# Kernel optimization log

Hardware: AMD Instinct MI355X
Metric: run time of the kernel (lower is better)

Reference implementation:

```python
import jax, jax.numpy as jnp
import numpy as np

N, C, H, E = 10000, 128, 256, 320000
CUTOFF = 5.0
EPS = 1e-5


def _ln(x, g, b):
    mu = jnp.mean(x, axis=-1, keepdims=True)
    var = jnp.var(x, axis=-1, keepdims=True)
    return (x - mu) * jax.lax.rsqrt(var + EPS) * g + b


def setup_inputs() -> dict:
    key = jax.random.key(0)
    ks = jax.random.split(key, 24)

    def w(k, shape, fan_in):
        return (jax.random.normal(k, shape, dtype=jnp.float32) / np.sqrt(fan_in)).astype(jnp.float32)

    inp = {}
    inp["x"] = jax.random.normal(ks[0], (N, 3), dtype=jnp.float32)
    inp["h"] = jax.random.normal(ks[1], (N, C), dtype=jnp.float32)
    inp["edge_index"] = jax.random.randint(ks[2], (2, E), 0, N, dtype=jnp.int32)
    # edge_mlp: Linear(2C+1 -> H), SiLU, Linear(H -> H), SiLU
    inp["We1"] = w(ks[3], (2 * C + 1, H), 2 * C + 1); inp["be1"] = jnp.zeros((H,), jnp.float32)
    inp["We2"] = w(ks[4], (H, H), H);                inp["be2"] = jnp.zeros((H,), jnp.float32)
    # node_mlp: Linear(C+H -> H), SiLU, Linear(H -> C)
    inp["Wn1"] = w(ks[5], (C + H, H), C + H);        inp["bn1"] = jnp.zeros((H,), jnp.float32)
    inp["Wn2"] = w(ks[6], (H, C), H);                inp["bn2"] = jnp.zeros((C,), jnp.float32)
    # residual mlp: Linear(C -> H), SiLU, Dropout(eval), Linear(H -> C)
    inp["Wm1"] = w(ks[7], (C, H), C);                inp["bm1"] = jnp.zeros((H,), jnp.float32)
    inp["Wm2"] = w(ks[8], (H, C), H);                inp["bm2"] = jnp.zeros((C,), jnp.float32)
    # layernorms
    inp["g1"] = jnp.ones((C,), jnp.float32); inp["beta1"] = jnp.zeros((C,), jnp.float32)
    inp["g2"] = jnp.ones((C,), jnp.float32); inp["beta2"] = jnp.zeros((C,), jnp.float32)
    return inp


def reference(x, h, edge_index, We1, be1, We2, be2, Wn1, bn1, Wn2, bn2,
              Wm1, bm1, Wm2, bm2, g1, beta1, g2, beta2):
    row, col = edge_index[0], edge_index[1]

    h_res = h
    hn = _ln(h, g1, beta1)                              # [N, C]

    # ---- EGNN layer ----
    rel = x[row] - x[col]                               # [E, 3]
    dist = jnp.linalg.norm(rel, axis=-1, keepdims=True) # [E, 1]
    edge_in = jnp.concatenate([hn[row], hn[col], dist], axis=-1)  # [E, 2C+1]
    m = jax.nn.silu(edge_in @ We1 + be1)
    m = jax.nn.silu(m @ We2 + be2)                      # [E, H]

    d = dist[:, 0]
    Ccut = 0.5 * (jnp.cos(d * jnp.pi / CUTOFF) + 1.0)
    Ccut = Ccut * (d <= CUTOFF) * (d >= 0.0)
    m = m * Ccut[:, None]

    # mean-aggregate messages at target nodes (edge_index[1])
    sums = jax.ops.segment_sum(m, col, num_segments=N)          # [N, H]
    cnt = jax.ops.segment_sum(jnp.ones((m.shape[0],), m.dtype), col, num_segments=N)
    m_aggr = sums / jnp.maximum(cnt, 1.0)[:, None]

    hd = jax.nn.silu(jnp.concatenate([hn, m_aggr], axis=-1) @ Wn1 + bn1) @ Wn2 + bn2
    h_egnn = hn + hd

    h1 = h_res + h_egnn

    # ---- norm2 + MLP residual (dropout = identity in eval) ----
    h2 = _ln(h1, g2, beta2)
    h2 = jax.nn.silu(h2 @ Wm1 + bm1) @ Wm2 + bm2
    return h1 + h2
```

## Files before the change

### kernel.cpp

```cpp
#include <hip/hip_runtime.h>

#define NN 10000
#define CC 128
#define HH 256
#define EE 320000
#define ETILE 128
#define EBLOCKS 2500

typedef __bf16 bf16_t;
typedef __bf16 bf16x8 __attribute__((ext_vector_type(8)));
typedef __bf16 bf16x4 __attribute__((ext_vector_type(4)));
typedef float f32x4 __attribute__((ext_vector_type(4)));

__device__ __forceinline__ float silu_f(float v) {
#if __has_builtin(__builtin_amdgcn_rcpf)
  return v * __builtin_amdgcn_rcpf(1.0f + __expf(-v));
#else
  return v / (1.0f + __expf(-v));
#endif
}

template<int RE, int KD, int SA, int NT>
__device__ __forceinline__ void gemm_lg(const bf16_t* sAa, const bf16_t* __restrict__ BT,
                                        int nwavebase, int lr, int quad, f32x4 acc[RE][NT]) {
  for (int kk = 0; kk < KD; kk += 32) {
    bf16x8 a[RE]; bf16x8 b[NT];
#pragma unroll
    for (int re = 0; re < RE; re++)
      a[re] = *(const bf16x8*)(sAa + (re * 16 + lr) * SA + kk + quad * 8);
#pragma unroll
    for (int ce = 0; ce < NT; ce++)
      b[ce] = *(const bf16x8*)(BT + (size_t)(nwavebase + ce * 16 + lr) * KD + kk + quad * 8);
#pragma unroll
    for (int re = 0; re < RE; re++)
#pragma unroll
      for (int ce = 0; ce < NT; ce++)
        acc[re][ce] = __builtin_amdgcn_mfma_f32_16x16x32_bf16(a[re], b[ce], acc[re][ce], 0, 0, 0);
  }
}

__global__ __launch_bounds__(256) void prep_kernel(
    const float* __restrict__ We1, const float* __restrict__ We2,
    const float* __restrict__ Wn1, const float* __restrict__ Wn2,
    const float* __restrict__ Wm1, const float* __restrict__ Wm2,
    bf16_t* __restrict__ We1T, bf16_t* __restrict__ We2T,
    bf16_t* __restrict__ Wn1T, bf16_t* __restrict__ Wn2T,
    bf16_t* __restrict__ Wm1T, bf16_t* __restrict__ Wm2T) {
  int i = blockIdx.x * 256 + threadIdx.x;
  if (i < 327680) {
    const float* src; bf16_t* dst; int K, Nc, idx;
    if      (i < 65536)  { src = We1; dst = We1T; K = 256; Nc = 256; idx = i; }
    else if (i < 131072) { src = We2; dst = We2T; K = 256; Nc = 256; idx = i - 65536; }
    else if (i < 229376) { src = Wn1; dst = Wn1T; K = 384; Nc = 256; idx = i - 131072; }
    else if (i < 262144) { src = Wn2; dst = Wn2T; K = 256; Nc = 128; idx = i - 229376; }
    else if (i < 294912) { src = Wm1; dst = Wm1T; K = 128; Nc = 256; idx = i - 262144; }
    else                 { src = Wm2; dst = Wm2T; K = 256; Nc = 128; idx = i - 294912; }
    int n = idx / K, k = idx - n * K;
    dst[idx] = (bf16_t)src[(size_t)k * Nc + n];
  }
}

__global__ __launch_bounds__(256, 4) void node_pre_kernel(
    const float* __restrict__ h, const float* __restrict__ g1,
    const float* __restrict__ bt1,
    const bf16_t* __restrict__ We1T, const float* __restrict__ be1,
    bf16_t* __restrict__ hn16, bf16_t* __restrict__ PQ,
    const int* __restrict__ ei, int* __restrict__ cnt) {
  __shared__ __align__(16) bf16_t sHn[16 * 136];
  int tid = threadIdx.x;
  if (blockIdx.x >= 625) {
    int e = (blockIdx.x - 625) * 256 + tid;
    atomicAdd(&cnt[ei[EE + e]], 1);
    return;
  }
  int lane = tid & 63, wave = tid >> 6;
  int lr = lane & 15, quad = lane >> 4;
  int n0 = blockIdx.x * 16;

  {
    int node = tid >> 4, c0 = (tid & 15) * 8;
    size_t base = (size_t)(n0 + node) * CC;
    f32x4 u0 = *(const f32x4*)(h + base + c0);
    f32x4 u1 = *(const f32x4*)(h + base + c0 + 4);
    float s = 0.f, sq = 0.f;
#pragma unroll
    for (int j = 0; j < 4; j++) { s += u0[j] + u1[j]; sq += u0[j] * u0[j] + u1[j] * u1[j]; }
#pragma unroll
    for (int o = 8; o > 0; o >>= 1) { s += __shfl_xor(s, o); sq += __shfl_xor(sq, o); }
    float mu = s * (1.0f / CC);
    float var = sq * (1.0f / CC) - mu * mu;
    float rs = rsqrtf(var + 1e-5f);
    f32x4 gg0 = *(const f32x4*)(g1 + c0), gg1 = *(const f32x4*)(g1 + c0 + 4);
    f32x4 bb0 = *(const f32x4*)(bt1 + c0), bb1 = *(const f32x4*)(bt1 + c0 + 4);
    bf16x8 ov;
#pragma unroll
    for (int j = 0; j < 4; j++) {
      ov[j] = (bf16_t)((u0[j] - mu) * rs * gg0[j] + bb0[j]);
      ov[j + 4] = (bf16_t)((u1[j] - mu) * rs * gg1[j] + bb1[j]);
    }
    *(bf16x8*)(sHn + node * 136 + c0) = ov;
    *(bf16x8*)(hn16 + base + c0) = ov;
  }
  __syncthreads();

  bool isQ = wave >= 2;
  int rbase = (wave & 1) * 128;
  int koff = isQ ? 128 : 0;
  f32x4 zf = {0.f, 0.f, 0.f, 0.f};
  f32x4 acc[8];
#pragma unroll
  for (int i = 0; i < 8; i++) acc[i] = zf;
  for (int kk = 0; kk < 128; kk += 32) {
    bf16x8 b = *(const bf16x8*)(sHn + lr * 136 + kk + quad * 8);
    bf16x8 a[8];
#pragma unroll
    for (int re = 0; re < 8; re++)
      a[re] = *(const bf16x8*)(We1T + (size_t)(rbase + re * 16 + lr) * 256 + koff + kk + quad * 8);
#pragma unroll
    for (int re = 0; re < 8; re++)
      acc[re] = __builtin_amdgcn_mfma_f32_16x16x32_bf16(a[re], b, acc[re], 0, 0, 0);
  }
#pragma unroll
  for (int re = 0; re < 8; re++) {
    int cb = rbase + re * 16 + quad * 4;
    f32x4 bb = isQ ? zf : *(const f32x4*)(be1 + cb);
    bf16x4 o;
#pragma unroll
    for (int r = 0; r < 4; r++) o[r] = (bf16_t)(acc[re][r] + bb[r]);
    *(bf16x4*)(PQ + (size_t)(n0 + lr) * 512 + (isQ ? 256 : 0) + cb) = o;
  }
}

__global__ __launch_bounds__(1024) void scan_kernel(const int* __restrict__ cnt, int* __restrict__ cursor) {
  __shared__ int wsum[16];
  int tid = threadIdx.x, wave = tid >> 6, lane = tid & 63;
  int base = tid * 10;
  int v[10]; int S = 0;
#pragma unroll
  for (int j = 0; j < 10; j++) {
    int i = base + j;
    v[j] = (i < NN) ? cnt[i] : 0;
    S += v[j];
  }
  int s = S;
#pragma unroll
  for (int off = 1; off < 64; off <<= 1) { int t = __shfl_up(s, off); if (lane >= off) s += t; }
  if (lane == 63) wsum[wave] = s;
  __syncthreads();
  if (tid < 16) {
    int ws = wsum[tid];
#pragma unroll
    for (int off = 1; off < 16; off <<= 1) { int t = __shfl_up(ws, off); if (tid >= off) ws += t; }
    wsum[tid] = ws;
  }
  __syncthreads();
  int ex = ((wave > 0) ? wsum[wave - 1] : 0) + s - S;
#pragma unroll
  for (int j = 0; j < 10; j++) {
    int i = base + j;
    if (i < NN) cursor[i] = ex;
    ex += v[j];
  }
}

__global__ __launch_bounds__(256) void scatter_kernel(const int* __restrict__ ei,
                                                      const float* __restrict__ x,
                                                      int* __restrict__ cursor,
                                                      uint4* __restrict__ edat) {
  int e = blockIdx.x * 256 + threadIdx.x;
  int r = ei[e], c = ei[EE + e];
  float dx = x[3 * r] - x[3 * c];
  float dy = x[3 * r + 1] - x[3 * c + 1];
  float dz = x[3 * r + 2] - x[3 * c + 2];
  float d = sqrtf(dx * dx + dy * dy + dz * dz);
  float cc = (d <= 5.0f) ? 0.5f * (__cosf(d * 0.6283185307179586f) + 1.0f) : 0.0f;
  int pos = atomicAdd(&cursor[c], 1);
  uint4 v = {(unsigned)r, (unsigned)c, __float_as_uint(d), __float_as_uint(cc)};
  edat[pos] = v;
}

__global__ __launch_bounds__(512, 4) void edge_mlp_kernel(
    const uint4* __restrict__ edat, const bf16_t* __restrict__ PQ,
    const float* __restrict__ We1last,
    const bf16_t* __restrict__ We2T, const float* __restrict__ be2,
    float* __restrict__ sums) {
  __shared__ __align__(512) bf16_t sM1[ETILE * 256];
  __shared__ int sRow[ETILE], sCol[ETILE];
  __shared__ float sD[ETILE], sCc[ETILE];
  __shared__ unsigned long long sMaskA, sMaskB;
  int tid = threadIdx.x;
  int lane = tid & 63, wave = tid >> 6;
  int lr = lane & 15, quad = lane >> 4;

  int bid = blockIdx.x;
  int xcd = bid & 7, rank = bid >> 3;
  int swz = (xcd < 4 ? xcd * 313 : 4 * 313 + (xcd - 4) * 312) + rank;
  int e0 = swz * ETILE;

  if (tid < ETILE) {
    uint4 v = edat[e0 + tid];
    sRow[tid] = (int)v.x; sCol[tid] = (int)v.y;
    sD[tid] = __uint_as_float(v.z); sCc[tid] = __uint_as_float(v.w);
  }
  __syncthreads();

  if (tid < ETILE) {
    int fl = (tid > 0) && (sCol[tid] != sCol[tid - 1]);
    unsigned long long m = __ballot(fl);
    if (tid == 0) sMaskA = m;
    if (tid == 64) sMaskB = m;
  }

#pragma unroll
  for (int i = 0; i < 8; i++) {
    int o = tid + i * 512;
    int e = o >> 5, q = o & 31;
    int k0 = q * 8;
    int row = sRow[e], col = sCol[e];
    float d = sD[e];
    bf16x8 pv = *(const bf16x8*)(PQ + (size_t)row * 512 + k0);
    bf16x8 qv = *(const bf16x8*)(PQ + (size_t)col * 512 + 256 + k0);
    f32x4 wl0 = *(const f32x4*)(We1last + k0);
    f32x4 wl1 = *(const f32x4*)(We1last + k0 + 4);
    bf16x8 m;
#pragma unroll
    for (int j = 0; j < 4; j++) {
      m[j] = (bf16_t)silu_f((float)pv[j] + (float)qv[j] + d * wl0[j]);
      m[j + 4] = (bf16_t)silu_f((float)pv[j + 4] + (float)qv[j + 4] + d * wl1[j]);
    }
    int boff = ((e << 9) + (q << 4)) ^ ((e & 7) << 4);
    *(bf16x8*)((char*)sM1 + boff) = m;
  }
  __syncthreads();

  f32x4 zf = {0.f, 0.f, 0.f, 0.f};
  f32x4 acc[8][2];
#pragma unroll
  for (int i = 0; i < 8; i++)
#pragma unroll
    for (int j = 0; j < 2; j++) acc[i][j] = zf;
  {
    int nb = wave * 32;
    for (int kk = 0; kk < 256; kk += 32) {
      bf16x8 a[8], b[2];
#pragma unroll
      for (int re = 0; re < 8; re++) {
        int row = re * 16 + lr;
        int boff = ((row << 9) + (kk << 1) + (quad << 4)) ^ ((row & 7) << 4);
        a[re] = *(const bf16x8*)((const char*)sM1 + boff);
      }
#pragma unroll
      for (int ce = 0; ce < 2; ce++)
        b[ce] = *(const bf16x8*)(We2T + (size_t)(nb + ce * 16 + lr) * 256 + kk + quad * 8);
#pragma unroll
      for (int re = 0; re < 8; re++)
#pragma unroll
        for (int ce = 0; ce < 2; ce++)
          acc[re][ce] = __builtin_amdgcn_mfma_f32_16x16x32_bf16(a[re], b[ce], acc[re][ce], 0, 0, 0);
    }
  }

  float be2v[2];
#pragma unroll
  for (int ce = 0; ce < 2; ce++) be2v[ce] = be2[wave * 32 + ce * 16 + lr];
#pragma unroll
  for (int re = 0; re < 8; re++) {
    f32x4 cc = *(const f32x4*)(sCc + re * 16 + quad * 4);
#pragma unroll
    for (int ce = 0; ce < 2; ce++)
#pragma unroll
      for (int r = 0; r < 4; r++)
        acc[re][ce][r] = silu_f(acc[re][ce][r] + be2v[ce]) * cc[r];
  }

  {
    unsigned long long mA = sMaskA;
    unsigned long long mB = sMaskB;
    int lo = 0;
    while (lo < ETILE) {
      int hi;
      if (lo < 63) {
        unsigned long long t = mA & (~0ull << (lo + 1));
        hi = t ? (__ffsll((long long)t) - 1)
               : (mB ? 64 + __ffsll((long long)mB) - 1 : ETILE);
      } else {
        int rel = lo - 64;
        unsigned long long t = (rel < 63) ? (mB & (~0ull << (rel + 1))) : 0ull;
        hi = t ? 64 + __ffsll((long long)t) - 1 : ETILE;
      }
      f32x4 tv = zf;
#pragma unroll
      for (int re = 0; re < 8; re++) {
        int t0 = re * 16, t1e = t0 + 16;
        if (t1e <= lo || t0 >= hi) continue;
        if (t0 >= lo && t1e <= hi) {
#pragma unroll
          for (int r = 0; r < 4; r++)
#pragma unroll
            for (int ce = 0; ce < 2; ce++)
              tv[ce] += acc[re][ce][r];
        } else {
          int eb = t0 + quad * 4;
#pragma unroll
          for (int r = 0; r < 4; r++) {
            int e = eb + r;
            bool in = (e >= lo) && (e < hi);
#pragma unroll
            for (int ce = 0; ce < 2; ce++)
              tv[ce] += in ? acc[re][ce][r] : 0.0f;
          }
        }
      }
#pragma unroll
      for (int ce = 0; ce < 2; ce++) {
        tv[ce] += __shfl_xor(tv[ce], 16);
        tv[ce] += __shfl_xor(tv[ce], 32);
      }
      if (quad == 0) {
        int colv = sCol[lo];
#pragma unroll
        for (int ce = 0; ce < 2; ce++)
          atomicAdd(&sums[(size_t)colv * HH + wave * 32 + ce * 16 + lr], tv[ce]);
      }
      lo = hi;
    }
  }
}

__global__ __launch_bounds__(256, 3) void node_fused_kernel(
    const float* __restrict__ h, const bf16_t* __restrict__ hn16,
    const float* __restrict__ sums, const int* __restrict__ cnt,
    const bf16_t* __restrict__ Wn1T, const float* __restrict__ bn1,
    const bf16_t* __restrict__ Wn2T, const float* __restrict__ bn2,
    const float* __restrict__ g2, const float* __restrict__ bt2,
    const bf16_t* __restrict__ Wm1T, const float* __restrict__ bm1,
    const bf16_t* __restrict__ Wm2T, const float* __restrict__ bm2,
    float* __restrict__ out) {
  __shared__ __align__(16) bf16_t sA1[16 * 392];
  __shared__ __align__(16) bf16_t sM[16 * 264];
  __shared__ __align__(16) float sH1[16 * 132];
  __shared__ __align__(16) bf16_t sLn[16 * 136];
  __shared__ float sRc[16];
  int tid = threadIdx.x;
  int lane = tid & 63, wave = tid >> 6;
  int lr = lane & 15, quad = lane >> 4;
  int n0 = blockIdx.x * 16;

  if (tid < 16) sRc[tid] = 1.0f / fmaxf((float)cnt[n0 + tid], 1.0f);
  __syncthreads();

#pragma unroll
  for (int i = 0; i < 3; i++) {
    int o = tid + i * 256;
    int e = o / 48, q = o - e * 48;
    int node = n0 + e;
    if (q < 16) {
      *(uint4*)(sA1 + e * 392 + q * 8) = *(const uint4*)(hn16 + (size_t)node * CC + q * 8);
    } else {
      float rc = sRc[e];
      const float* sp = sums + (size_t)node * HH + (q - 16) * 8;
      bf16x8 bv;
#pragma unroll
      for (int k2 = 0; k2 < 8; k2++) bv[k2] = (bf16_t)(sp[k2] * rc);
      *(bf16x8*)(sA1 + e * 392 + 128 + (q - 16) * 8) = bv;
    }
  }
  __syncthreads();

  f32x4 zf = {0.f, 0.f, 0.f, 0.f};
  {
    f32x4 acc[1][4];
#pragma unroll
    for (int j = 0; j < 4; j++) acc[0][j] = zf;
    gemm_lg<1, 384, 392, 4>(sA1, Wn1T, wave * 64, lr, quad, acc);
#pragma unroll
    for (int ce = 0; ce < 4; ce++) {
      int n = wave * 64 + ce * 16 + lr;
      float b1 = bn1[n];
#pragma unroll
      for (int r = 0; r < 4; r++)
        sM[(quad * 4 + r) * 264 + n] = (bf16_t)silu_f(acc[0][ce][r] + b1);
    }
  }
  __syncthreads();

  {
    f32x4 acc[1][2];
    acc[0][0] = zf; acc[0][1] = zf;
    gemm_lg<1, 256, 264, 2>(sM, Wn2T, wave * 32, lr, quad, acc);
#pragma unroll
    for (int ce = 0; ce < 2; ce++) {
      int n = wave * 32 + ce * 16 + lr;
      float b2 = bn2[n];
#pragma unroll
      for (int r = 0; r < 4; r++) {
        int node = quad * 4 + r;
        size_t idx = (size_t)(n0 + node) * CC + n;
        float hn_v = (float)sA1[node * 392 + n];
        sH1[node * 132 + n] = h[idx] + hn_v + acc[0][ce][r] + b2;
      }
    }
  }
  __syncthreads();

  {
    int node = tid >> 4, c0 = (tid & 15) * 8;
    f32x4 u0 = *(const f32x4*)(sH1 + node * 132 + c0);
    f32x4 u1 = *(const f32x4*)(sH1 + node * 132 + c0 + 4);
    float s = 0.f, sq = 0.f;
#pragma unroll
    for (int j = 0; j < 4; j++) { s += u0[j] + u1[j]; sq += u0[j] * u0[j] + u1[j] * u1[j]; }
#pragma unroll
    for (int o = 8; o > 0; o >>= 1) { s += __shfl_xor(s, o); sq += __shfl_xor(sq, o); }
    float mu = s * (1.0f / CC);
    float var = sq * (1.0f / CC) - mu * mu;
    float rs = rsqrtf(var + 1e-5f);
    f32x4 gg0 = *(const f32x4*)(g2 + c0), gg1 = *(const f32x4*)(g2 + c0 + 4);
    f32x4 bb0 = *(const f32x4*)(bt2 + c0), bb1 = *(const f32x4*)(bt2 + c0 + 4);
    bf16x8 ov;
#pragma unroll
    for (int j = 0; j < 4; j++) {
      ov[j] = (bf16_t)((u0[j] - mu) * rs * gg0[j] + bb0[j]);
      ov[j + 4] = (bf16_t)((u1[j] - mu) * rs * gg1[j] + bb1[j]);
    }
    *(bf16x8*)(sLn + node * 136 + c0) = ov;
  }
  __syncthreads();

  {
    f32x4 acc[1][4];
#pragma unroll
    for (int j = 0; j < 4; j++) acc[0][j] = zf;
    gemm_lg<1, 128, 136, 4>(sLn, Wm1T, wave * 64, lr, quad, acc);
#pragma unroll
    for (int ce = 0; ce < 4; ce++) {
      int n = wave * 64 + ce * 16 + lr;
      float b1 = bm1[n];
#pragma unroll
      for (int r = 0; r < 4; r++)
        sM[(quad * 4 + r) * 264 + n] = (bf16_t)silu_f(acc[0][ce][r] + b1);
    }
  }
  __syncthreads();

  {
    f32x4 acc[1][2];
    acc[0][0] = zf; acc[0][1] = zf;
    gemm_lg<1, 256, 264, 2>(sM, Wm2T, wave * 32, lr, quad, acc);
#pragma unroll
    for (int ce = 0; ce < 2; ce++) {
      int n = wave * 32 + ce * 16 + lr;
      float b2 = bm2[n];
#pragma unroll
      for (int r = 0; r < 4; r++) {
        int node = quad * 4 + r;
        size_t idx = (size_t)(n0 + node) * CC + n;
        out[idx] = sH1[node * 132 + n] + acc[0][ce][r] + b2;
      }
    }
  }
}

extern "C" void kernel_launch(void* const* d_in, const int* in_sizes, int n_in,
                              void* d_out, int out_size, void* d_ws, size_t ws_size,
                              hipStream_t stream) {
  const float* x    = (const float*)d_in[0];
  const float* h    = (const float*)d_in[1];
  const int*   ei   = (const int*)d_in[2];
  const float* We1  = (const float*)d_in[3];
  const float* be1  = (const float*)d_in[4];
  const float* We2  = (const float*)d_in[5];
  const float* be2  = (const float*)d_in[6];
  const float* Wn1  = (const float*)d_in[7];
  const float* bn1  = (const float*)d_in[8];
  const float* Wn2  = (const float*)d_in[9];
  const float* bn2  = (const float*)d_in[10];
  const float* Wm1  = (const float*)d_in[11];
  const float* bm1  = (const float*)d_in[12];
  const float* Wm2  = (const float*)d_in[13];
  const float* bm2  = (const float*)d_in[14];
  const float* g1   = (const float*)d_in[15];
  const float* bt1  = (const float*)d_in[16];
  const float* g2   = (const float*)d_in[17];
  const float* bt2  = (const float*)d_in[18];
  float* out = (float*)d_out;

  char* wp = (char*)d_ws;
  size_t off = 0;
  auto alloc = [&](size_t bytes) -> void* {
    void* p = wp + off;
    off = (off + bytes + 255) & ~(size_t)255;
    return p;
  };

  bf16_t* hn16   = (bf16_t*)alloc((size_t)NN * CC * 2);
  bf16_t* PQ     = (bf16_t*)alloc((size_t)NN * 512 * 2);
  float*  sums   = (float*)alloc((size_t)NN * HH * 4);
  int*    cnt    = (int*)alloc((size_t)NN * 4);
  int*    cursor = (int*)alloc((size_t)NN * 4);
  uint4*  edat   = (uint4*)alloc((size_t)EE * 16);
  bf16_t* We1T   = (bf16_t*)alloc(256 * 256 * 2);
  bf16_t* We2T   = (bf16_t*)alloc(256 * 256 * 2);
  bf16_t* Wn1T   = (bf16_t*)alloc(256 * 384 * 2);
  bf16_t* Wn2T   = (bf16_t*)alloc(128 * 256 * 2);
  bf16_t* Wm1T   = (bf16_t*)alloc(256 * 128 * 2);
  bf16_t* Wm2T   = (bf16_t*)alloc(128 * 256 * 2);

  hipMemsetAsync(sums, 0, (size_t)NN * HH * 4, stream);
  hipMemsetAsync(cnt, 0, (size_t)NN * 4, stream);

  prep_kernel<<<1280, 256, 0, stream>>>(We1, We2, Wn1, Wn2, Wm1, Wm2,
                                        We1T, We2T, Wn1T, Wn2T, Wm1T, Wm2T);

  node_pre_kernel<<<1875, 256, 0, stream>>>(h, g1, bt1, We1T, be1, hn16, PQ,
                                            ei, cnt);

  scan_kernel<<<1, 1024, 0, stream>>>(cnt, cursor);
  scatter_kernel<<<EE / 256, 256, 0, stream>>>(ei, x, cursor, edat);

  edge_mlp_kernel<<<EBLOCKS, 512, 0, stream>>>(edat, PQ, We1 + 256 * 256,
                                               We2T, be2, sums);

  node_fused_kernel<<<NN / 16, 256, 0, stream>>>(h, hn16, sums, cnt,
                                                 Wn1T, bn1, Wn2T, bn2,
                                                 g2, bt2, Wm1T, bm1, Wm2T, bm2, out);
}
```

Measured before the change: 296.4 us.

## Make edge MLP kernel persistent with double-buffered tiles and register-resident We2

The edge MLP kernel becomes a persistent grid of 256 blocks that loop over edge tiles. It double-buffers the edge metadata and the first-layer activation tile in shared memory and prefetches the next tile's PQ gathers into registers while the current tile's MFMA and segmented atomics run. We2T fragments are loaded once into registers per block instead of on every tile. The trade-off is more register and LDS pressure (occupancy hint drops from 4 to 2), only 256 blocks for the whole device, and the loss of the previous XCD-aware tile swizzle.

```diff
diff --git a/kernel.cpp b/kernel.cpp
--- a/kernel.cpp
+++ b/kernel.cpp
@@ -6,6 +6,7 @@
 #define EE 320000
 #define ETILE 128
 #define EBLOCKS 2500
+#define PBLOCKS 256
 
 typedef __bf16 bf16_t;
 typedef __bf16 bf16x8 __attribute__((ext_vector_type(8)));
@@ -179,151 +180,180 @@
   edat[pos] = v;
 }
 
-__global__ __launch_bounds__(512, 4) void edge_mlp_kernel(
+__global__ __launch_bounds__(512, 2) void edge_mlp_kernel(
     const uint4* __restrict__ edat, const bf16_t* __restrict__ PQ,
     const float* __restrict__ We1last,
     const bf16_t* __restrict__ We2T, const float* __restrict__ be2,
     float* __restrict__ sums) {
-  __shared__ __align__(512) bf16_t sM1[ETILE * 256];
-  __shared__ int sRow[ETILE], sCol[ETILE];
-  __shared__ float sD[ETILE], sCc[ETILE];
-  __shared__ unsigned long long sMaskA, sMaskB;
+  __shared__ __align__(512) bf16_t sM1[2][ETILE * 256];
+  __shared__ int sRow[2][ETILE], sCol[2][ETILE];
+  __shared__ float sD[2][ETILE], sCc[2][ETILE];
+  __shared__ unsigned long long sMaskA[2], sMaskB[2];
   int tid = threadIdx.x;
   int lane = tid & 63, wave = tid >> 6;
   int lr = lane & 15, quad = lane >> 4;
-
-  int bid = blockIdx.x;
-  int xcd = bid & 7, rank = bid >> 3;
-  int swz = (xcd < 4 ? xcd * 313 : 4 * 313 + (xcd - 4) * 312) + rank;
-  int e0 = swz * ETILE;
+  int ebase = tid >> 5;
+  int k0 = (tid & 31) * 8;
+  int nb = wave * 32;
+
+  bf16x8 breg[8][2];
+#pragma unroll
+  for (int k8 = 0; k8 < 8; k8++)
+#pragma unroll
+    for (int ce = 0; ce < 2; ce++)
+      breg[k8][ce] = *(const bf16x8*)(We2T + (size_t)(nb + ce * 16 + lr) * 256 + k8 * 32 + quad * 8);
+
+  f32x4 wl0 = *(const f32x4*)(We1last + k0);
+  f32x4 wl1 = *(const f32x4*)(We1last + k0 + 4);
+  float be2v[2];
+  be2v[0] = be2[nb + lr];
+  be2v[1] = be2[nb + 16 + lr];
+
+  int t0 = blockIdx.x;
+  int cur = 0;
 
   if (tid < ETILE) {
-    uint4 v = edat[e0 + tid];
-    sRow[tid] = (int)v.x; sCol[tid] = (int)v.y;
-    sD[tid] = __uint_as_float(v.z); sCc[tid] = __uint_as_float(v.w);
-  }
-  __syncthreads();
-
+    uint4 v = edat[(size_t)t0 * ETILE + tid];
+    sRow[0][tid] = (int)v.x; sCol[0][tid] = (int)v.y;
+    sD[0][tid] = __uint_as_float(v.z); sCc[0][tid] = __uint_as_float(v.w);
+  }
+  __syncthreads();
   if (tid < ETILE) {
-    int fl = (tid > 0) && (sCol[tid] != sCol[tid - 1]);
+    int fl = (tid > 0) && (sCol[0][tid] != sCol[0][tid - 1]);
     unsigned long long m = __ballot(fl);
-    if (tid == 0) sMaskA = m;
-    if (tid == 64) sMaskB = m;
-  }
-
+    if (tid == 0) sMaskA[0] = m;
+    if (tid == 64) sMaskB[0] = m;
+  }
+  bf16x8 pv[8], qv[8];
 #pragma unroll
   for (int i = 0; i < 8; i++) {
-    int o = tid + i * 512;
-    int e = o >> 5, q = o & 31;
-    int k0 = q * 8;
-    int row = sRow[e], col = sCol[e];
-    float d = sD[e];
-    bf16x8 pv = *(const bf16x8*)(PQ + (size_t)row * 512 + k0);
-    bf16x8 qv = *(const bf16x8*)(PQ + (size_t)col * 512 + 256 + k0);
-    f32x4 wl0 = *(const f32x4*)(We1last + k0);
-    f32x4 wl1 = *(const f32x4*)(We1last + k0 + 4);
-    bf16x8 m;
-#pragma unroll
-    for (int j = 0; j < 4; j++) {
-      m[j] = (bf16_t)silu_f((float)pv[j] + (float)qv[j] + d * wl0[j]);
-      m[j + 4] = (bf16_t)silu_f((float)pv[j + 4] + (float)qv[j + 4] + d * wl1[j]);
-    }
-    int boff = ((e << 9) + (q << 4)) ^ ((e & 7) << 4);
-    *(bf16x8*)((char*)sM1 + boff) = m;
-  }
-  __syncthreads();
+    int e = ebase + i * 16;
+    pv[i] = *(const bf16x8*)(PQ + (size_t)sRow[0][e] * 512 + k0);
+    qv[i] = *(const bf16x8*)(PQ + (size_t)sCol[0][e] * 512 + 256 + k0);
+  }
 
   f32x4 zf = {0.f, 0.f, 0.f, 0.f};
-  f32x4 acc[8][2];
-#pragma unroll
-  for (int i = 0; i < 8; i++)
-#pragma unroll
-    for (int j = 0; j < 2; j++) acc[i][j] = zf;
-  {
-    int nb = wave * 32;
-    for (int kk = 0; kk < 256; kk += 32) {
-      bf16x8 a[8], b[2];
+  for (int t = t0; t < EBLOCKS; t += PBLOCKS) {
+    int nxt = cur ^ 1;
+    bool haveNext = (t + PBLOCKS) < EBLOCKS;
+
+    if (haveNext && tid < ETILE) {
+      uint4 v = edat[(size_t)(t + PBLOCKS) * ETILE + tid];
+      sRow[nxt][tid] = (int)v.x; sCol[nxt][tid] = (int)v.y;
+      sD[nxt][tid] = __uint_as_float(v.z); sCc[nxt][tid] = __uint_as_float(v.w);
+    }
+#pragma unroll
+    for (int i = 0; i < 8; i++) {
+      int e = ebase + i * 16;
+      float d = sD[cur][e];
+      bf16x8 m;
+#pragma unroll
+      for (int j = 0; j < 4; j++) {
+        m[j]     = (bf16_t)silu_f((float)pv[i][j] + (float)qv[i][j] + d * wl0[j]);
+        m[j + 4] = (bf16_t)silu_f((float)pv[i][j + 4] + (float)qv[i][j + 4] + d * wl1[j]);
+      }
+      int boff = ((e << 9) + (k0 << 1)) ^ ((e & 7) << 4);
+      *(bf16x8*)((char*)sM1[cur] + boff) = m;
+    }
+    __syncthreads();
+
+    if (haveNext && tid < ETILE) {
+      int fl = (tid > 0) && (sCol[nxt][tid] != sCol[nxt][tid - 1]);
+      unsigned long long mm = __ballot(fl);
+      if (tid == 0) sMaskA[nxt] = mm;
+      if (tid == 64) sMaskB[nxt] = mm;
+    }
+    if (haveNext) {
+#pragma unroll
+      for (int i = 0; i < 8; i++) {
+        int e = ebase + i * 16;
+        pv[i] = *(const bf16x8*)(PQ + (size_t)sRow[nxt][e] * 512 + k0);
+        qv[i] = *(const bf16x8*)(PQ + (size_t)sCol[nxt][e] * 512 + 256 + k0);
+      }
+    }
+
+    f32x4 acc[8][2];
+#pragma unroll
+    for (int i = 0; i < 8; i++) { acc[i][0] = zf; acc[i][1] = zf; }
+    for (int k8 = 0; k8 < 8; k8++) {
+      bf16x8 a[8];
 #pragma unroll
       for (int re = 0; re < 8; re++) {
         int row = re * 16 + lr;
-        int boff = ((row << 9) + (kk << 1) + (quad << 4)) ^ ((row & 7) << 4);
-        a[re] = *(const bf16x8*)((const char*)sM1 + boff);
+        int boff = ((row << 9) + (k8 << 6) + (quad << 4)) ^ ((row & 7) << 4);
+        a[re] = *(const bf16x8*)((const char*)sM1[cur] + boff);
       }
 #pragma unroll
+      for (int re = 0; re < 8; re++)
+#pragma unroll
+        for (int ce = 0; ce < 2; ce++)
+          acc[re][ce] = __builtin_amdgcn_mfma_f32_16x16x32_bf16(a[re], breg[k8][ce], acc[re][ce], 0, 0, 0);
+    }
+
+#pragma unroll
+    for (int re = 0; re < 8; re++) {
+      f32x4 cc = *(const f32x4*)(&sCc[cur][re * 16 + quad * 4]);
+#pragma unroll
       for (int ce = 0; ce < 2; ce++)
-        b[ce] = *(const bf16x8*)(We2T + (size_t)(nb + ce * 16 + lr) * 256 + kk + quad * 8);
-#pragma unroll
-      for (int re = 0; re < 8; re++)
-#pragma unroll
-        for (int ce = 0; ce < 2; ce++)
-          acc[re][ce] = __builtin_amdgcn_mfma_f32_16x16x32_bf16(a[re], b[ce], acc[re][ce], 0, 0, 0);
-    }
-  }
-
-  float be2v[2];
-#pragma unroll
-  for (int ce = 0; ce < 2; ce++) be2v[ce] = be2[wave * 32 + ce * 16 + lr];
-#pragma unroll
-  for (int re = 0; re < 8; re++) {
-    f32x4 cc = *(const f32x4*)(sCc + re * 16 + quad * 4);
-#pragma unroll
-    for (int ce = 0; ce < 2; ce++)
-#pragma unroll
-      for (int r = 0; r < 4; r++)
-        acc[re][ce][r] = silu_f(acc[re][ce][r] + be2v[ce]) * cc[r];
-  }
-
-  {
-    unsigned long long mA = sMaskA;
-    unsigned long long mB = sMaskB;
-    int lo = 0;
-    while (lo < ETILE) {
-      int hi;
-      if (lo < 63) {
-        unsigned long long t = mA & (~0ull << (lo + 1));
-        hi = t ? (__ffsll((long long)t) - 1)
-               : (mB ? 64 + __ffsll((long long)mB) - 1 : ETILE);
-      } else {
-        int rel = lo - 64;
-        unsigned long long t = (rel < 63) ? (mB & (~0ull << (rel + 1))) : 0ull;
-        hi = t ? 64 + __ffsll((long long)t) - 1 : ETILE;
-      }
-      f32x4 tv = zf;
-#pragma unroll
-      for (int re = 0; re < 8; re++) {
-        int t0 = re * 16, t1e = t0 + 16;
-        if (t1e <= lo || t0 >= hi) continue;
-        if (t0 >= lo && t1e <= hi) {
-#pragma unroll
-          for (int r = 0; r < 4; r++)
-#pragma unroll
-            for (int ce = 0; ce < 2; ce++)
-              tv[ce] += acc[re][ce][r];
+#pragma unroll
+        for (int r = 0; r < 4; r++)
+          acc[re][ce][r] = silu_f(acc[re][ce][r] + be2v[ce]) * cc[r];
+    }
+
+    {
+      unsigned long long mA = sMaskA[cur];
+      unsigned long long mB = sMaskB[cur];
+      int lo = 0;
+      while (lo < ETILE) {
+        int hi;
+        if (lo < 63) {
+          unsigned long long tt = mA & (~0ull << (lo + 1));
+          hi = tt ? (__ffsll((long long)tt) - 1)
+                  : (mB ? 64 + __ffsll((long long)mB) - 1 : ETILE);
         } else {
-          int eb = t0 + quad * 4;
-#pragma unroll
-          for (int r = 0; r < 4; r++) {
-            int e = eb + r;
-            bool in = (e >= lo) && (e < hi);
-#pragma unroll
-            for (int ce = 0; ce < 2; ce++)
-              tv[ce] += in ? acc[re][ce][r] : 0.0f;
+          int rel = lo - 64;
+          unsigned long long tt = (rel < 63) ? (mB & (~0ull << (rel + 1))) : 0ull;
+          hi = tt ? 64 + __ffsll((long long)tt) - 1 : ETILE;
+        }
+        f32x4 tv = zf;
+#pragma unroll
+        for (int re = 0; re < 8; re++) {
+          int tA = re * 16, tE = tA + 16;
+          if (tE <= lo || tA >= hi) continue;
+          if (tA >= lo && tE <= hi) {
+#pragma unroll
+            for (int r = 0; r < 4; r++)
+#pragma unroll
+              for (int ce = 0; ce < 2; ce++)
+                tv[ce] += acc[re][ce][r];
+          } else {
+            int eb = tA + quad * 4;
+#pragma unroll
+            for (int r = 0; r < 4; r++) {
+              int e = eb + r;
+              bool in = (e >= lo) && (e < hi);
+#pragma unroll
+              for (int ce = 0; ce < 2; ce++)
+                tv[ce] += in ? acc[re][ce][r] : 0.0f;
+            }
           }
         }
+#pragma unroll
+        for (int ce = 0; ce < 2; ce++) {
+          tv[ce] += __shfl_xor(tv[ce], 16);
+          tv[ce] += __shfl_xor(tv[ce], 32);
+        }
+        if (quad == 0) {
+          int colv = sCol[cur][lo];
+#pragma unroll
+          for (int ce = 0; ce < 2; ce++)
+            atomicAdd(&sums[(size_t)colv * HH + nb + ce * 16 + lr], tv[ce]);
+        }
+        lo = hi;
       }
-#pragma unroll
-      for (int ce = 0; ce < 2; ce++) {
-        tv[ce] += __shfl_xor(tv[ce], 16);
-        tv[ce] += __shfl_xor(tv[ce], 32);
-      }
-      if (quad == 0) {
-        int colv = sCol[lo];
-#pragma unroll
-        for (int ce = 0; ce < 2; ce++)
-          atomicAdd(&sums[(size_t)colv * HH + wave * 32 + ce * 16 + lr], tv[ce]);
-      }
-      lo = hi;
-    }
+    }
+    __syncthreads();
+    cur ^= 1;
   }
 }
 
@@ -518,7 +548,7 @@
   scan_kernel<<<1, 1024, 0, stream>>>(cnt, cursor);
   scatter_kernel<<<EE / 256, 256, 0, stream>>>(ei, x, cursor, edat);
 
-  edge_mlp_kernel<<<EBLOCKS, 512, 0, stream>>>(edat, PQ, We1 + 256 * 256,
+  edge_mlp_kernel<<<PBLOCKS, 512, 0, stream>>>(edat, PQ, We1 + 256 * 256,
                                                We2T, be2, sums);
 
   node_fused_kernel<<<NN / 16, 256, 0, stream>>>(h, hn16, sums, cnt,
```

Result: slower. 507.2 us (+71.1%).
